# Performance work log

Hardware: AMD Instinct MI355X
Metric: run time of the kernel (lower is better)

## Reference

```python
import jax, jax.numpy as jnp
import numpy as np

N_NODES = 100000; N_RELS = 100; EMB = 128; HID = 768; LAYERS = 12
CW = 3; HEADS = 12; DH = HID // HEADS; FF = 4 * HID
B = 256; S = 128


def _statics():
    # Sliding-window mask from build_mask(): rows with offset <= S-L get the
    # submask [0]*2cw + [-inf] + [0]*2cw at [offset:offset+L]; remaining rows
    # are all -inf (we neutralize those rows to avoid NaN; their attn output
    # is zeroed, see VALID).
    Lw = 4 * CW + 1
    r = np.arange(S)[:, None]; c = np.arange(S)[None, :]
    valid = np.arange(S) <= S - Lw
    inwin = (c >= r) & (c < r + Lw) & (c != r + 2 * CW) & valid[:, None]
    addmask = np.where(inwin, 0.0, -np.inf).astype(np.float32)
    addmask = np.where(valid[:, None], addmask, 0.0)
    ri, ci = np.nonzero(inwin)  # selection indices for pos_dist[:, mask]
    # sinusoidal positional encoding (S, HID)
    pos = np.arange(S)[:, None].astype(np.float32)
    div = np.exp(-np.log(10000.0) * np.arange(0, HID, 2) / HID)
    pe = np.zeros((S, HID), np.float32)
    pe[:, 0::2] = np.sin(pos * div); pe[:, 1::2] = np.cos(pos * div)
    return (jnp.asarray(addmask), jnp.asarray(valid), jnp.asarray(ri),
            jnp.asarray(ci), jnp.asarray(pe))

ADDMASK, VALID, RI, CI, PE = _statics()


def _ln(x, g, b, eps=1e-5):
    m = jnp.mean(x, -1, keepdims=True)
    v = jnp.mean((x - m) ** 2, -1, keepdims=True)
    return (x - m) * jax.lax.rsqrt(v + eps) * g + b


def setup_inputs() -> dict:
    key = jax.random.key(0)
    ks = iter(jax.random.split(key, 40))
    nrm = lambda shp, s=0.02: jax.random.normal(next(ks), shp, jnp.float32) * s
    V = N_NODES + N_RELS
    d = {}
    d['seq'] = jax.random.randint(next(ks), (B, S), 0, V, jnp.int32)
    d['neg_idx'] = jax.random.randint(next(ks), (B, S), 0, N_NODES, jnp.int32)
    d['embed_W'] = nrm((V, EMB), 1.0)
    d['embed_g'] = jnp.ones((EMB,)); d['embed_b'] = jnp.zeros((EMB,))
    d['proj_W'] = nrm((EMB, HID)); d['proj_b'] = jnp.zeros((HID,))
    d['qkv_W'] = nrm((LAYERS, HID, 3 * HID)); d['qkv_b'] = jnp.zeros((LAYERS, 3 * HID))
    d['ao_W'] = nrm((LAYERS, HID, HID)); d['ao_b'] = jnp.zeros((LAYERS, HID))
    d['ln1_g'] = jnp.ones((LAYERS, HID)); d['ln1_b'] = jnp.zeros((LAYERS, HID))
    d['ff1_W'] = nrm((LAYERS, HID, FF)); d['ff1_b'] = jnp.zeros((LAYERS, FF))
    d['ff2_W'] = nrm((LAYERS, FF, HID)); d['ff2_b'] = jnp.zeros((LAYERS, HID))
    d['ln2_g'] = jnp.ones((LAYERS, HID)); d['ln2_b'] = jnp.zeros((LAYERS, HID))
    d['head_W'] = nrm((HID, EMB)); d['head_b'] = jnp.zeros((EMB,))
    d['head_g'] = jnp.ones((EMB,)); d['head_beta'] = jnp.zeros((EMB,))
    d['oemb_W'] = nrm((V, EMB), 1.0)
    d['oemb_g'] = jnp.ones((EMB,)); d['oemb_b'] = jnp.zeros((EMB,))
    return d


def reference(seq, neg_idx, embed_W, embed_g, embed_b, proj_W, proj_b,
              qkv_W, qkv_b, ao_W, ao_b, ln1_g, ln1_b, ff1_W, ff1_b,
              ff2_W, ff2_b, ln2_g, ln2_b, head_W, head_b, head_g, head_beta,
              oemb_W, oemb_g, oemb_b):
    b, s = seq.shape
    z = _ln(embed_W[seq], embed_g, embed_b)                 # (B,S,E)
    x = jax.nn.gelu(z @ proj_W + proj_b, approximate=False)  # (B,S,H)
    x = x + PE[None, :, :]
    vrow = VALID.astype(x.dtype)[None, None, :, None]

    def layer(x, p):
        qkv = x @ p['qw'] + p['qb']
        q, k, v = jnp.split(qkv, 3, axis=-1)
        q = q.reshape(b, s, HEADS, DH); k = k.reshape(b, s, HEADS, DH)
        v = v.reshape(b, s, HEADS, DH)
        scores = jnp.einsum('bihd,bjhd->bhij', q, k) / np.sqrt(DH)
        attn = jax.nn.softmax(scores + ADDMASK, axis=-1) * vrow
        ctx = jnp.einsum('bhij,bjhd->bihd', attn, v).reshape(b, s, HID)
        x = _ln(x + ctx @ p['aw'] + p['ab'], p['g1'], p['b1'])
        h = jax.nn.gelu(x @ p['f1w'] + p['f1b'], approximate=False)
        x = _ln(x + h @ p['f2w'] + p['f2b'], p['g2'], p['b2'])
        return x, None

    params = {'qw': qkv_W, 'qb': qkv_b, 'aw': ao_W, 'ab': ao_b,
              'g1': ln1_g, 'b1': ln1_b, 'f1w': ff1_W, 'f1b': ff1_b,
              'f2w': ff2_W, 'f2b': ff2_b, 'g2': ln2_g, 'b2': ln2_b}
    x, _ = jax.lax.scan(layer, x, params)

    preds = _ln(x @ head_W + head_b, head_g, head_beta)     # (B,S,E)
    out_z = _ln(oemb_W[seq], oemb_g, oemb_b)                # (B,S,E)
    pos_dist = jnp.einsum('bie,bje->bij', out_z, preds)     # (B,S,S)
    pos = pos_dist[:, RI, CI].reshape(-1, 2 * CW).mean(-1)
    neg_e = _ln(oemb_W[neg_idx], oemb_g, oemb_b)
    neg_dist = jnp.einsum('bie,bje->bij', out_z, neg_e)
    neg = neg_dist[:, RI, CI].reshape(-1, 2 * CW).mean(-1)
    # BCEWithLogitsLoss: labels 1 for pos, 0 for neg, mean reduction
    n = pos.shape[0] + neg.shape[0]
    loss = (jnp.sum(jax.nn.softplus(-pos)) + jnp.sum(jax.nn.softplus(neg))) / n
    return loss
```

## Files before the change

### kernel.cpp

```cpp
#include <hip/hip_runtime.h>
#include <hip/hip_bf16.h>

typedef __hip_bfloat16 bf16;
typedef __bf16 bf16x8 __attribute__((ext_vector_type(8)));
typedef float f32x4 __attribute__((ext_vector_type(4)));

#define B_      256
#define S_      128
#define HID_    768
#define EMB_    128
#define FF_     3072
#define LAYERS_ 12
#define HEADS_  12
#define DH_     64
#define M_TOK   (B_ * S_)

__device__ inline float b2f(bf16 v) { return __bfloat162float(v); }
__device__ inline bf16  f2b(float v) { return __float2bfloat16(v); }

__device__ inline float wave_sum(float v) {
#pragma unroll
  for (int o = 32; o > 0; o >>= 1) v += __shfl_xor(v, o, 64);
  return v;
}

__device__ inline float gelu_exact(float x) {
  return 0.5f * x * (1.0f + erff(x * 0.70710678118654752f));
}

__device__ inline void glds16(const bf16* g, bf16* l) {
  __builtin_amdgcn_global_load_lds(
      (const __attribute__((address_space(1))) void*)g,
      (__attribute__((address_space(3))) void*)l, 16, 0, 0);
}

__device__ inline void bar()   { asm volatile("s_barrier" ::: "memory"); }
__device__ inline void lgkm0() {
  asm volatile("s_waitcnt lgkmcnt(0)" ::: "memory");
  __builtin_amdgcn_sched_barrier(0);
}

__global__ __launch_bounds__(512, 2)
void gemm256(const bf16* __restrict__ A, const bf16* __restrict__ Bt,
             const float* __restrict__ bias, bf16* __restrict__ C,
             int M, int N, int K, int mode)
{
  __shared__ __align__(16) bf16 As[2][256 * 64];
  __shared__ __align__(16) bf16 Bs[2][256 * 64];
  const int tid  = threadIdx.x;
  const int w    = tid >> 6, lane = tid & 63;
  const int wm   = w >> 2,  wn   = w & 3;

  const int nwg = gridDim.x * gridDim.y;
  int bid = blockIdx.y * gridDim.x + blockIdx.x;
  {
    const int q = nwg >> 3, r = nwg & 7, xcd = bid & 7, off = bid >> 3;
    bid = (xcd < r ? xcd * (q + 1) : r * (q + 1) + (xcd - r) * q) + off;
  }
  const int m0 = (bid / gridDim.x) * 256;
  const int n0 = (bid % gridDim.x) * 256;

  const int NT = K >> 6;

  const int c0   = w * 2;
  const int srow = c0 * 8 + (lane >> 3);
  const int scol = ((lane & 7) ^ (lane >> 3)) * 8;
  const bf16* gA0 = A  + (size_t)(m0 + srow)     * K + scol;
  const bf16* gA1 = A  + (size_t)(m0 + srow + 8) * K + scol;
  const bf16* gB0 = Bt + (size_t)(n0 + srow)     * K + scol;
  const bf16* gB1 = Bt + (size_t)(n0 + srow + 8) * K + scol;

  auto stageA = [&](int bi, int h, int kt) {
    const size_t go = (size_t)h * 128 * (size_t)K + (size_t)kt * 64;
    bf16* l = &As[bi][h * 8192 + c0 * 512];
    glds16(gA0 + go, l);
    glds16(gA1 + go, l + 512);
  };
  auto stageB = [&](int bi, int h, int kt) {
    const size_t go = (size_t)h * 128 * (size_t)K + (size_t)kt * 64;
    bf16* l = &Bs[bi][h * 8192 + c0 * 512];
    glds16(gB0 + go, l);
    glds16(gB1 + go, l + 512);
  };

  const int lr = lane & 15, lk = (lane >> 4) * 8, sx = (lane & 7) << 3;
  auto rdA = [&](int bi, int f, int kk) -> bf16x8 {
    return *(const bf16x8*)&As[bi][((f * 32 + wm * 16 + lr) * 64 + kk * 32 + lk) ^ sx];
  };
  auto rdB = [&](int bi, int g, int kk) -> bf16x8 {
    return *(const bf16x8*)&Bs[bi][((g * 64 + wn * 16 + lr) * 64 + kk * 32 + lk) ^ sx];
  };

  const f32x4 zacc = {0.f, 0.f, 0.f, 0.f};
  f32x4 acc[8][4];
#pragma unroll
  for (int f = 0; f < 8; f++)
#pragma unroll
    for (int g = 0; g < 4; g++) acc[f][g] = zacc;

  stageA(0, 0, 0);
  stageB(0, 1, 0);
  stageB(0, 0, 0);
  stageA(0, 1, 0);
  if (NT > 1) { stageA(1, 0, 1); stageB(1, 1, 1); }
  asm volatile("s_waitcnt vmcnt(4)" ::: "memory");
  bar();

  for (int kt = 0; kt < NT; ++kt) {
    const int bi = kt & 1, nb = bi ^ 1;
    bf16x8 af[4][2], b01[2][2], b23[2][2];

#pragma unroll
    for (int f = 0; f < 4; f++) { af[f][0] = rdA(bi, f, 0); af[f][1] = rdA(bi, f, 1); }
#pragma unroll
    for (int g = 0; g < 2; g++) { b01[g][0] = rdB(bi, g, 0); b01[g][1] = rdB(bi, g, 1); }
    if (kt + 1 < NT) stageB(nb, 0, kt + 1);
    bar(); lgkm0();
    __builtin_amdgcn_s_setprio(1);
#pragma unroll
    for (int f = 0; f < 4; f++)
#pragma unroll
      for (int g = 0; g < 2; g++) {
        acc[f][g] = __builtin_amdgcn_mfma_f32_16x16x32_bf16(af[f][0], b01[g][0], acc[f][g], 0, 0, 0);
        acc[f][g] = __builtin_amdgcn_mfma_f32_16x16x32_bf16(af[f][1], b01[g][1], acc[f][g], 0, 0, 0);
      }
    __builtin_amdgcn_s_setprio(0);
    bar();

#pragma unroll
    for (int g = 0; g < 2; g++) { b23[g][0] = rdB(bi, g + 2, 0); b23[g][1] = rdB(bi, g + 2, 1); }
    if (kt + 1 < NT) stageA(nb, 1, kt + 1);
    bar(); lgkm0();
    __builtin_amdgcn_s_setprio(1);
#pragma unroll
    for (int f = 0; f < 4; f++)
#pragma unroll
      for (int g = 0; g < 2; g++) {
        acc[f][g + 2] = __builtin_amdgcn_mfma_f32_16x16x32_bf16(af[f][0], b23[g][0], acc[f][g + 2], 0, 0, 0);
        acc[f][g + 2] = __builtin_amdgcn_mfma_f32_16x16x32_bf16(af[f][1], b23[g][1], acc[f][g + 2], 0, 0, 0);
      }
    __builtin_amdgcn_s_setprio(0);
    bar();

#pragma unroll
    for (int f = 0; f < 4; f++) { af[f][0] = rdA(bi, f + 4, 0); af[f][1] = rdA(bi, f + 4, 1); }
    if (kt + 2 < NT) stageA(bi, 0, kt + 2);
    bar(); lgkm0();
    __builtin_amdgcn_s_setprio(1);
#pragma unroll
    for (int f = 0; f < 4; f++)
#pragma unroll
      for (int g = 0; g < 2; g++) {
        acc[f + 4][g + 2] = __builtin_amdgcn_mfma_f32_16x16x32_bf16(af[f][0], b23[g][0], acc[f + 4][g + 2], 0, 0, 0);
        acc[f + 4][g + 2] = __builtin_amdgcn_mfma_f32_16x16x32_bf16(af[f][1], b23[g][1], acc[f + 4][g + 2], 0, 0, 0);
      }
    __builtin_amdgcn_s_setprio(0);
    bar();

    if (kt + 2 < NT) stageB(bi, 1, kt + 2);
    if (kt < NT - 2) asm volatile("s_waitcnt vmcnt(4)" ::: "memory");
    else             asm volatile("s_waitcnt vmcnt(0)" ::: "memory");
    bar();
    __builtin_amdgcn_s_setprio(1);
#pragma unroll
    for (int f = 0; f < 4; f++)
#pragma unroll
      for (int g = 0; g < 2; g++) {
        acc[f + 4][g] = __builtin_amdgcn_mfma_f32_16x16x32_bf16(af[f][0], b01[g][0], acc[f + 4][g], 0, 0, 0);
        acc[f + 4][g] = __builtin_amdgcn_mfma_f32_16x16x32_bf16(af[f][1], b01[g][1], acc[f + 4][g], 0, 0, 0);
      }
    __builtin_amdgcn_s_setprio(0);
    bar();
  }

  const int er = (lane >> 4) * 4, ec = lane & 15;
#pragma unroll
  for (int f = 0; f < 8; f++) {
    const int row = m0 + f * 32 + wm * 16 + er;
#pragma unroll
    for (int g = 0; g < 4; g++) {
      const int col = n0 + g * 64 + wn * 16 + ec;
      const float bv = bias[col];
#pragma unroll
      for (int r = 0; r < 4; r++) {
        float v = acc[f][g][r] + bv;
        if (mode >= 1) v = gelu_exact(v);
        C[(size_t)(row + r) * N + col] = f2b(v);
      }
    }
  }
}

__global__ __launch_bounds__(256)
void gemm_bt(const bf16* __restrict__ A, const bf16* __restrict__ Bt,
             const float* __restrict__ bias, bf16* __restrict__ C,
             int M, int N, int K, int mode)
{
  __shared__ __align__(16) bf16 As[128 * 32];
  __shared__ __align__(16) bf16 Bs[128 * 32];
  const int tid  = threadIdx.x;
  const int wave = tid >> 6, lane = tid & 63;
  const int m0 = blockIdx.y * 128, n0 = blockIdx.x * 128;

  const int ar = lane >> 2;
  const int ac = (lane & 3) * 8;
  const int c0 = wave * 2;
  const bf16* ga0 = A  + (size_t)(m0 + c0 * 16      + ar) * K + ac;
  const bf16* ga1 = A  + (size_t)(m0 + (c0+1) * 16  + ar) * K + ac;
  const bf16* gb0 = Bt + (size_t)(n0 + c0 * 16      + ar) * K + ac;
  const bf16* gb1 = Bt + (size_t)(n0 + (c0+1) * 16  + ar) * K + ac;
  bf16* lA0 = As + c0 * 512;       bf16* lA1 = As + (c0 + 1) * 512;
  bf16* lB0 = Bs + c0 * 512;       bf16* lB1 = Bs + (c0 + 1) * 512;

  const int lr = lane & 15;
  const int lk = (lane >> 4) * 8;
  const int rm = (wave >> 1) * 64;
  const int rn = (wave & 1) * 64;

  const f32x4 zacc = {0.f, 0.f, 0.f, 0.f};
  f32x4 acc[4][4];
#pragma unroll
  for (int i = 0; i < 4; i++)
#pragma unroll
    for (int j = 0; j < 4; j++) acc[i][j] = zacc;

  for (int k0 = 0; k0 < K; k0 += 32) {
    glds16(ga0 + k0, lA0);
    glds16(ga1 + k0, lA1);
    glds16(gb0 + k0, lB0);
    glds16(gb1 + k0, lB1);
    __syncthreads();
    bf16x8 af[4], bfr[4];
#pragma unroll
    for (int i = 0; i < 4; i++) af[i]  = *(const bf16x8*)&As[(rm + i * 16 + lr) * 32 + lk];
#pragma unroll
    for (int j = 0; j < 4; j++) bfr[j] = *(const bf16x8*)&Bs[(rn + j * 16 + lr) * 32 + lk];
#pragma unroll
    for (int i = 0; i < 4; i++)
#pragma unroll
      for (int j = 0; j < 4; j++)
        acc[i][j] = __builtin_amdgcn_mfma_f32_16x16x32_bf16(af[i], bfr[j], acc[i][j], 0, 0, 0);
    __syncthreads();
  }

  const int er = (lane >> 4) * 4;
  const int ec = lane & 15;
#pragma unroll
  for (int i = 0; i < 4; i++) {
    const int row = m0 + rm + i * 16 + er;
#pragma unroll
    for (int j = 0; j < 4; j++) {
      const int col = n0 + rn + j * 16 + ec;
      const float bv = bias[col];
#pragma unroll
      for (int r = 0; r < 4; r++) {
        float v = acc[i][j][r] + bv;
        if (mode >= 1) v = gelu_exact(v);
        if (mode == 2) {
          const int srow = (row + r) & (S_ - 1);
          const int i2 = col & ~1;
          const float div = expf(-9.210340371976184f * (float)i2 * (1.0f / (float)HID_));
          const float ang = (float)srow * div;
          v += (col & 1) ? cosf(ang) : sinf(ang);
        }
        C[(size_t)(row + r) * N + col] = f2b(v);
      }
    }
  }
}

__global__ __launch_bounds__(256)
void convtrans(const float* __restrict__ src, bf16* __restrict__ dst, int K, int N)
{
  __shared__ bf16 t[32][33];
  const int n0 = blockIdx.x * 32, k0 = blockIdx.y * 32;
  const int tx = threadIdx.x, ty = threadIdx.y;
#pragma unroll
  for (int i = 0; i < 4; i++)
    t[ty + i * 8][tx] = f2b(src[(size_t)(k0 + ty + i * 8) * N + n0 + tx]);
  __syncthreads();
#pragma unroll
  for (int i = 0; i < 4; i++)
    dst[(size_t)(n0 + ty + i * 8) * K + k0 + tx] = t[tx][ty + i * 8];
}

__global__ __launch_bounds__(128)
void attn_kernel(const bf16* __restrict__ qkv, bf16* __restrict__ ctx)
{
  const int bh = blockIdx.x;
  const int b = bh / HEADS_, h = bh % HEADS_;
  __shared__ __align__(16) bf16 qs[S_ * DH_];
  __shared__ __align__(16) bf16 ks[S_ * DH_];
  __shared__ __align__(16) bf16 vs[S_ * DH_];
  const int tid = threadIdx.x;
  const bf16* base = qkv + (size_t)b * S_ * (3 * HID_) + h * DH_;
  for (int it = 0; it < 8; ++it) {
    const int s = it * 16 + (tid >> 3);
    const int seg = (tid & 7) * 8;
    const size_t go = (size_t)s * (3 * HID_) + seg;
    *(uint4*)&qs[s * DH_ + seg] = *(const uint4*)&base[go];
    *(uint4*)&ks[s * DH_ + seg] = *(const uint4*)&base[go + HID_];
    *(uint4*)&vs[s * DH_ + seg] = *(const uint4*)&base[go + 2 * HID_];
  }
  __syncthreads();
  const int i = tid;
  bf16* out = ctx + (size_t)(b * S_ + i) * HID_ + h * DH_;
  if (i < 116) {
    float p[13];
    float mx = -1e30f;
    for (int jj = 0; jj < 13; jj++) {
      if (jj == 6) { p[jj] = 0.f; continue; }
      float d = 0.f;
#pragma unroll
      for (int dd = 0; dd < DH_; dd++) d += b2f(qs[i * DH_ + dd]) * b2f(ks[(i + jj) * DH_ + dd]);
      p[jj] = d * 0.125f;
      mx = fmaxf(mx, p[jj]);
    }
    float l = 0.f;
    for (int jj = 0; jj < 13; jj++) {
      if (jj == 6) { p[jj] = 0.f; continue; }
      p[jj] = expf(p[jj] - mx);
      l += p[jj];
    }
    const float inv = 1.f / l;
    float o[DH_];
#pragma unroll
    for (int dd = 0; dd < DH_; dd++) o[dd] = 0.f;
    for (int jj = 0; jj < 13; jj++) {
      if (jj == 6) continue;
      const float pj = p[jj] * inv;
#pragma unroll
      for (int dd = 0; dd < DH_; dd++) o[dd] += pj * b2f(vs[(i + jj) * DH_ + dd]);
    }
#pragma unroll
    for (int dd = 0; dd < DH_; dd++) out[dd] = f2b(o[dd]);
  } else {
#pragma unroll
    for (int dd = 0; dd < DH_; dd++) out[dd] = f2b(0.f);
  }
}

__global__ __launch_bounds__(256)
void add_ln_kernel(const bf16* __restrict__ x, const bf16* __restrict__ y,
                   const float* __restrict__ g, const float* __restrict__ bta,
                   bf16* __restrict__ out)
{
  const int r = blockIdx.x, tid = threadIdx.x;
  const size_t base = (size_t)r * HID_;
  float v[3];
#pragma unroll
  for (int e = 0; e < 3; e++) {
    const int idx = tid + e * 256;
    v[e] = b2f(x[base + idx]) + b2f(y[base + idx]);
  }
  float s  = v[0] + v[1] + v[2];
  float ss = v[0] * v[0] + v[1] * v[1] + v[2] * v[2];
  s = wave_sum(s);
  ss = wave_sum(ss);
  __shared__ float red[8];
  const int wave = tid >> 6, lane = tid & 63;
  if (lane == 0) { red[wave] = s; red[4 + wave] = ss; }
  __syncthreads();
  s  = red[0] + red[1] + red[2] + red[3];
  ss = red[4] + red[5] + red[6] + red[7];
  const float mean = s * (1.f / (float)HID_);
  const float var  = ss * (1.f / (float)HID_) - mean * mean;
  const float rs = rsqrtf(var + 1e-5f);
#pragma unroll
  for (int e = 0; e < 3; e++) {
    const int idx = tid + e * 256;
    out[base + idx] = f2b((v[e] - mean) * rs * g[idx] + bta[idx]);
  }
}

__global__ __launch_bounds__(256)
void gather_ln128(const int* __restrict__ idx, const float* __restrict__ W,
                  const float* __restrict__ g, const float* __restrict__ bta,
                  bf16* __restrict__ out)
{
  const int token = blockIdx.x * 4 + (threadIdx.x >> 6);
  const int lane = threadIdx.x & 63;
  const int row = idx[token];
  const float* src = W + (size_t)row * 128;
  const float a = src[lane], c = src[lane + 64];
  const float s  = wave_sum(a + c);
  const float ss = wave_sum(a * a + c * c);
  const float mean = s * (1.f / 128.f);
  const float var  = ss * (1.f / 128.f) - mean * mean;
  const float rs = rsqrtf(var + 1e-5f);
  bf16* o = out + (size_t)token * 128;
  o[lane]      = f2b((a - mean) * rs * g[lane] + bta[lane]);
  o[lane + 64] = f2b((c - mean) * rs * g[lane + 64] + bta[lane + 64]);
}

__global__ __launch_bounds__(256)
void ln128_bf16(const bf16* __restrict__ in, const float* __restrict__ g,
                const float* __restrict__ bta, bf16* __restrict__ out)
{
  const int token = blockIdx.x * 4 + (threadIdx.x >> 6);
  const int lane = threadIdx.x & 63;
  const bf16* src = in + (size_t)token * 128;
  const float a = b2f(src[lane]), c = b2f(src[lane + 64]);
  const float s  = wave_sum(a + c);
  const float ss = wave_sum(a * a + c * c);
  const float mean = s * (1.f / 128.f);
  const float var  = ss * (1.f / 128.f) - mean * mean;
  const float rs = rsqrtf(var + 1e-5f);
  bf16* o = out + (size_t)token * 128;
  o[lane]      = f2b((a - mean) * rs * g[lane] + bta[lane]);
  o[lane + 64] = f2b((c - mean) * rs * g[lane + 64] + bta[lane + 64]);
}

__global__ __launch_bounds__(256)
void loss_kernel(const bf16* __restrict__ out_z, const bf16* __restrict__ preds,
                 const bf16* __restrict__ neg_e, float* __restrict__ out)
{
  const int b = blockIdx.x;
  const int which = blockIdx.y;
  __shared__ __align__(16) bf16 zo[128 * 128];
  __shared__ __align__(16) bf16 mt[128 * 128];
  const bf16* msrc = which ? neg_e : preds;
  const uint4* gz = (const uint4*)(out_z + (size_t)b * 16384);
  const uint4* gm = (const uint4*)(msrc + (size_t)b * 16384);
  for (int it = threadIdx.x; it < 2048; it += 256) {
    ((uint4*)zo)[it] = gz[it];
    ((uint4*)mt)[it] = gm[it];
  }
  __syncthreads();
  float local = 0.f;
  for (int it = threadIdx.x; it < 232; it += 256) {
    const int i = it >> 1;
    const int sub = it & 1;
    const int c0 = i + (sub ? 7 : 0);
    const bf16* zr = &zo[i * 128];
    float accv = 0.f;
    for (int jj = 0; jj < 6; jj++) {
      const bf16* mr = &mt[(c0 + jj) * 128];
      float d = 0.f;
#pragma unroll
      for (int dd = 0; dd < 128; dd++) d += b2f(zr[dd]) * b2f(mr[dd]);
      accv += d;
    }
    const float mean = accv * (1.f / 6.f);
    const float xin = which ? mean : -mean;
    local += fmaxf(xin, 0.f) + log1pf(expf(-fabsf(xin)));
  }
  local = wave_sum(local);
  if ((threadIdx.x & 63) == 0)
    atomicAdd(out, local * (1.f / 118784.f));
}

__global__ void zero_kernel(float* p) { p[0] = 0.f; }

extern "C" void kernel_launch(void* const* d_in, const int* in_sizes, int n_in,
                              void* d_out, int out_size, void* d_ws, size_t ws_size,
                              hipStream_t stream)
{
  (void)in_sizes; (void)n_in; (void)out_size; (void)ws_size;
  const int*   seq     = (const int*)  d_in[0];
  const int*   neg_idx = (const int*)  d_in[1];
  const float* embed_W = (const float*)d_in[2];
  const float* embed_g = (const float*)d_in[3];
  const float* embed_b = (const float*)d_in[4];
  const float* proj_W  = (const float*)d_in[5];
  const float* proj_b  = (const float*)d_in[6];
  const float* qkv_W   = (const float*)d_in[7];
  const float* qkv_b   = (const float*)d_in[8];
  const float* ao_W    = (const float*)d_in[9];
  const float* ao_b    = (const float*)d_in[10];
  const float* ln1_g   = (const float*)d_in[11];
  const float* ln1_b   = (const float*)d_in[12];
  const float* ff1_W   = (const float*)d_in[13];
  const float* ff1_b   = (const float*)d_in[14];
  const float* ff2_W   = (const float*)d_in[15];
  const float* ff2_b   = (const float*)d_in[16];
  const float* ln2_g   = (const float*)d_in[17];
  const float* ln2_b   = (const float*)d_in[18];
  const float* head_W  = (const float*)d_in[19];
  const float* head_b  = (const float*)d_in[20];
  const float* head_g  = (const float*)d_in[21];
  const float* head_bt = (const float*)d_in[22];
  const float* oemb_W  = (const float*)d_in[23];
  const float* oemb_g  = (const float*)d_in[24];
  const float* oemb_b  = (const float*)d_in[25];
  float* out = (float*)d_out;

  char* ws = (char*)d_ws;
  size_t off = 0;
  auto alloc = [&](size_t bytes) -> char* {
    char* p = ws + off;
    off += (bytes + 255) & ~(size_t)255;
    return p;
  };
  bf16* wt_qkv  = (bf16*)alloc((size_t)2304 * 768 * 2);
  bf16* wt_ao   = (bf16*)alloc((size_t)768 * 768 * 2);
  bf16* wt_ff1  = (bf16*)alloc((size_t)3072 * 768 * 2);
  bf16* wt_ff2  = (bf16*)alloc((size_t)768 * 3072 * 2);
  bf16* wt_proj = (bf16*)alloc((size_t)768 * 128 * 2);
  bf16* wt_head = (bf16*)alloc((size_t)128 * 768 * 2);
  bf16* zbuf    = (bf16*)alloc((size_t)M_TOK * 128 * 2);
  bf16* x       = (bf16*)alloc((size_t)M_TOK * 768 * 2);
  bf16* big     = (bf16*)alloc((size_t)M_TOK * 3072 * 2);
  bf16* ctx     = (bf16*)alloc((size_t)M_TOK * 768 * 2);
  bf16* ybuf    = (bf16*)alloc((size_t)M_TOK * 768 * 2);
  bf16* p0      = (bf16*)alloc((size_t)M_TOK * 128 * 2);
  bf16* preds   = (bf16*)alloc((size_t)M_TOK * 128 * 2);
  bf16* outz    = (bf16*)alloc((size_t)M_TOK * 128 * 2);
  bf16* nege    = (bf16*)alloc((size_t)M_TOK * 128 * 2);

  const dim3 tb(32, 8);

  convtrans<<<dim3(768 / 32, 128 / 32), tb, 0, stream>>>(proj_W, wt_proj, 128, 768);
  convtrans<<<dim3(128 / 32, 768 / 32), tb, 0, stream>>>(head_W, wt_head, 768, 128);

  gather_ln128<<<M_TOK / 4, 256, 0, stream>>>(seq, embed_W, embed_g, embed_b, zbuf);
  gemm_bt<<<dim3(768 / 128, M_TOK / 128), 256, 0, stream>>>(zbuf, wt_proj, proj_b, x,
                                                            M_TOK, 768, 128, 2);

  for (int l = 0; l < LAYERS_; ++l) {
    convtrans<<<dim3(2304 / 32, 768 / 32), tb, 0, stream>>>(qkv_W + (size_t)l * 768 * 2304, wt_qkv, 768, 2304);
    convtrans<<<dim3(768 / 32, 768 / 32), tb, 0, stream>>>(ao_W + (size_t)l * 768 * 768, wt_ao, 768, 768);
    convtrans<<<dim3(3072 / 32, 768 / 32), tb, 0, stream>>>(ff1_W + (size_t)l * 768 * 3072, wt_ff1, 768, 3072);
    convtrans<<<dim3(768 / 32, 3072 / 32), tb, 0, stream>>>(ff2_W + (size_t)l * 3072 * 768, wt_ff2, 3072, 768);

    gemm256<<<dim3(2304 / 256, M_TOK / 256), 512, 0, stream>>>(x, wt_qkv, qkv_b + l * 2304, big,
                                                               M_TOK, 2304, 768, 0);
    attn_kernel<<<B_ * HEADS_, 128, 0, stream>>>(big, ctx);
    gemm256<<<dim3(768 / 256, M_TOK / 256), 512, 0, stream>>>(ctx, wt_ao, ao_b + l * 768, ybuf,
                                                              M_TOK, 768, 768, 0);
    add_ln_kernel<<<M_TOK, 256, 0, stream>>>(x, ybuf, ln1_g + l * 768, ln1_b + l * 768, x);
    gemm256<<<dim3(3072 / 256, M_TOK / 256), 512, 0, stream>>>(x, wt_ff1, ff1_b + l * 3072, big,
                                                               M_TOK, 3072, 768, 1);
    gemm256<<<dim3(768 / 256, M_TOK / 256), 512, 0, stream>>>(big, wt_ff2, ff2_b + l * 768, ybuf,
                                                              M_TOK, 768, 3072, 0);
    add_ln_kernel<<<M_TOK, 256, 0, stream>>>(x, ybuf, ln2_g + l * 768, ln2_b + l * 768, x);
  }

  gemm_bt<<<dim3(1, M_TOK / 128), 256, 0, stream>>>(x, wt_head, head_b, p0, M_TOK, 128, 768, 0);
  ln128_bf16<<<M_TOK / 4, 256, 0, stream>>>(p0, head_g, head_bt, preds);
  gather_ln128<<<M_TOK / 4, 256, 0, stream>>>(seq, oemb_W, oemb_g, oemb_b, outz);
  gather_ln128<<<M_TOK / 4, 256, 0, stream>>>(neg_idx, oemb_W, oemb_g, oemb_b, nege);
  zero_kernel<<<1, 1, 0, stream>>>(out);
  loss_kernel<<<dim3(B_, 2), 256, 0, stream>>>(outz, preds, nege, out);
}
```

Before: 10.71 ms.

## Make GEMM persistent with cross-tile prefetch and use polynomial GELU approximation

Turns the 256x256 GEMM into a persistent kernel of 256 workgroups, each looping over several output tiles. The next tile's first k-slices are prefetched while the current tile finishes, so the pipeline does not drain between tiles, and launch tail effects shrink. It also replaces erff-based exact GELU with an Abramowitz-Stegun polynomial plus fast exp, which cuts epilogue cost but adds approximation error of roughly 1e-7 in erf. The tile split assumes the tile count divides evenly by 8 XCDs and 32 slots per XCD.

```diff
diff --git a/kernel.cpp b/kernel.cpp
--- a/kernel.cpp
+++ b/kernel.cpp
@@ -24,8 +24,19 @@
   return v;
 }
 
-__device__ inline float gelu_exact(float x) {
-  return 0.5f * x * (1.0f + erff(x * 0.70710678118654752f));
+__device__ inline float gelu_fast(float x) {
+  const float s  = x * 0.70710678118654752f;
+  const float ax = fabsf(s);
+  const float t  = 1.0f / fmaf(0.3275911f, ax, 1.0f);
+  float y = fmaf(t, 1.061405429f, -1.453152027f);
+  y = fmaf(t, y, 1.421413741f);
+  y = fmaf(t, y, -0.284496736f);
+  y = fmaf(t, y, 0.254829592f);
+  y = y * t;
+  const float e  = __expf(-ax * ax);
+  float er = 1.0f - y * e;
+  er = copysignf(er, s);
+  return 0.5f * x * (1.0f + er);
 }
 
 __device__ inline void glds16(const bf16* g, bf16* l) {
@@ -41,9 +52,9 @@
 }
 
 __global__ __launch_bounds__(512, 2)
-void gemm256(const bf16* __restrict__ A, const bf16* __restrict__ Bt,
-             const float* __restrict__ bias, bf16* __restrict__ C,
-             int M, int N, int K, int mode)
+void gemm256p(const bf16* __restrict__ A, const bf16* __restrict__ Bt,
+              const float* __restrict__ bias, bf16* __restrict__ C,
+              int M, int N, int K, int mode)
 {
   __shared__ __align__(16) bf16 As[2][256 * 64];
   __shared__ __align__(16) bf16 Bs[2][256 * 64];
@@ -51,36 +62,36 @@
   const int w    = tid >> 6, lane = tid & 63;
   const int wm   = w >> 2,  wn   = w & 3;
 
-  const int nwg = gridDim.x * gridDim.y;
-  int bid = blockIdx.y * gridDim.x + blockIdx.x;
-  {
-    const int q = nwg >> 3, r = nwg & 7, xcd = bid & 7, off = bid >> 3;
-    bid = (xcd < r ? xcd * (q + 1) : r * (q + 1) + (xcd - r) * q) + off;
-  }
-  const int m0 = (bid / gridDim.x) * 256;
-  const int n0 = (bid % gridDim.x) * 256;
-
+  const int gx  = N >> 8;
+  const int T   = (M >> 8) * gx;
+  const int Cx  = T >> 3;
+  const int xcd = blockIdx.x & 7, ci = blockIdx.x >> 3;
+  if (ci >= Cx) return;
+  const int R = (Cx - 1 - ci) / 32 + 1;
   const int NT = K >> 6;
+  const int U  = R * NT;
+
+  int jc = 0, kt = 0;
+  const int t0 = xcd * Cx + ci;
+  int m0 = (t0 / gx) << 8, n0 = (t0 % gx) << 8;
+  int m0n = 0, n0n = 0;
+  if (R > 1) { const int tn = t0 + 32; m0n = (tn / gx) << 8; n0n = (tn % gx) << 8; }
 
   const int c0   = w * 2;
   const int srow = c0 * 8 + (lane >> 3);
   const int scol = ((lane & 7) ^ (lane >> 3)) * 8;
-  const bf16* gA0 = A  + (size_t)(m0 + srow)     * K + scol;
-  const bf16* gA1 = A  + (size_t)(m0 + srow + 8) * K + scol;
-  const bf16* gB0 = Bt + (size_t)(n0 + srow)     * K + scol;
-  const bf16* gB1 = Bt + (size_t)(n0 + srow + 8) * K + scol;
-
-  auto stageA = [&](int bi, int h, int kt) {
-    const size_t go = (size_t)h * 128 * (size_t)K + (size_t)kt * 64;
+
+  auto stA = [&](int bi, int h, int m0t, int ktt) {
+    const bf16* g = A + (size_t)(m0t + h * 128 + srow) * K + (ktt * 64 + scol);
     bf16* l = &As[bi][h * 8192 + c0 * 512];
-    glds16(gA0 + go, l);
-    glds16(gA1 + go, l + 512);
+    glds16(g, l);
+    glds16(g + (size_t)8 * K, l + 512);
   };
-  auto stageB = [&](int bi, int h, int kt) {
-    const size_t go = (size_t)h * 128 * (size_t)K + (size_t)kt * 64;
+  auto stB = [&](int bi, int h, int n0t, int ktt) {
+    const bf16* g = Bt + (size_t)(n0t + h * 128 + srow) * K + (ktt * 64 + scol);
     bf16* l = &Bs[bi][h * 8192 + c0 * 512];
-    glds16(gB0 + go, l);
-    glds16(gB1 + go, l + 512);
+    glds16(g, l);
+    glds16(g + (size_t)8 * K, l + 512);
   };
 
   const int lr = lane & 15, lk = (lane >> 4) * 8, sx = (lane & 7) << 3;
@@ -98,23 +109,28 @@
 #pragma unroll
     for (int g = 0; g < 4; g++) acc[f][g] = zacc;
 
-  stageA(0, 0, 0);
-  stageB(0, 1, 0);
-  stageB(0, 0, 0);
-  stageA(0, 1, 0);
-  if (NT > 1) { stageA(1, 0, 1); stageB(1, 1, 1); }
+  const int er = (lane >> 4) * 4, ec = lane & 15;
+
+  stA(0, 0, m0, 0); stB(0, 1, n0, 0); stB(0, 0, n0, 0); stA(0, 1, m0, 0);
+  stA(1, 0, m0, 1); stB(1, 1, n0, 1);
   asm volatile("s_waitcnt vmcnt(4)" ::: "memory");
   bar();
 
-  for (int kt = 0; kt < NT; ++kt) {
-    const int bi = kt & 1, nb = bi ^ 1;
+  for (int u = 0; u < U; ++u) {
+    const int bi = u & 1, nb = bi ^ 1;
+    const bool h1 = (u + 1 < U), h2 = (u + 2 < U);
+    int kt1 = kt + 1, m01 = m0, n01 = n0;
+    if (kt1 == NT) { kt1 = 0; m01 = m0n; n01 = n0n; }
+    int kt2 = kt + 2, m02 = m0, n02 = n0;
+    if (kt2 >= NT) { kt2 -= NT; m02 = m0n; n02 = n0n; }
+
     bf16x8 af[4][2], b01[2][2], b23[2][2];
 
 #pragma unroll
     for (int f = 0; f < 4; f++) { af[f][0] = rdA(bi, f, 0); af[f][1] = rdA(bi, f, 1); }
 #pragma unroll
     for (int g = 0; g < 2; g++) { b01[g][0] = rdB(bi, g, 0); b01[g][1] = rdB(bi, g, 1); }
-    if (kt + 1 < NT) stageB(nb, 0, kt + 1);
+    if (h1) stB(nb, 0, n01, kt1);
     bar(); lgkm0();
     __builtin_amdgcn_s_setprio(1);
 #pragma unroll
@@ -129,7 +145,7 @@
 
 #pragma unroll
     for (int g = 0; g < 2; g++) { b23[g][0] = rdB(bi, g + 2, 0); b23[g][1] = rdB(bi, g + 2, 1); }
-    if (kt + 1 < NT) stageA(nb, 1, kt + 1);
+    if (h1) stA(nb, 1, m01, kt1);
     bar(); lgkm0();
     __builtin_amdgcn_s_setprio(1);
 #pragma unroll
@@ -144,7 +160,7 @@
 
 #pragma unroll
     for (int f = 0; f < 4; f++) { af[f][0] = rdA(bi, f + 4, 0); af[f][1] = rdA(bi, f + 4, 1); }
-    if (kt + 2 < NT) stageA(bi, 0, kt + 2);
+    if (h2) stA(bi, 0, m02, kt2);
     bar(); lgkm0();
     __builtin_amdgcn_s_setprio(1);
 #pragma unroll
@@ -157,9 +173,9 @@
     __builtin_amdgcn_s_setprio(0);
     bar();
 
-    if (kt + 2 < NT) stageB(bi, 1, kt + 2);
-    if (kt < NT - 2) asm volatile("s_waitcnt vmcnt(4)" ::: "memory");
-    else             asm volatile("s_waitcnt vmcnt(0)" ::: "memory");
+    if (h2) stB(bi, 1, n02, kt2);
+    if (u < U - 2) asm volatile("s_waitcnt vmcnt(4)" ::: "memory");
+    else           asm volatile("s_waitcnt vmcnt(0)" ::: "memory");
     bar();
     __builtin_amdgcn_s_setprio(1);
 #pragma unroll
@@ -171,21 +187,29 @@
       }
     __builtin_amdgcn_s_setprio(0);
     bar();
-  }
-
-  const int er = (lane >> 4) * 4, ec = lane & 15;
-#pragma unroll
-  for (int f = 0; f < 8; f++) {
-    const int row = m0 + f * 32 + wm * 16 + er;
-#pragma unroll
-    for (int g = 0; g < 4; g++) {
-      const int col = n0 + g * 64 + wn * 16 + ec;
-      const float bv = bias[col];
-#pragma unroll
-      for (int r = 0; r < 4; r++) {
-        float v = acc[f][g][r] + bv;
-        if (mode >= 1) v = gelu_exact(v);
-        C[(size_t)(row + r) * N + col] = f2b(v);
+
+    if (++kt == NT) {
+#pragma unroll
+      for (int f = 0; f < 8; f++) {
+        const int row = m0 + f * 32 + wm * 16 + er;
+#pragma unroll
+        for (int g = 0; g < 4; g++) {
+          const int col = n0 + g * 64 + wn * 16 + ec;
+          const float bv = bias[col];
+#pragma unroll
+          for (int r = 0; r < 4; r++) {
+            float v = acc[f][g][r] + bv;
+            if (mode >= 1) v = gelu_fast(v);
+            C[(size_t)(row + r) * N + col] = f2b(v);
+          }
+          acc[f][g] = zacc;
+        }
+      }
+      kt = 0; ++jc;
+      m0 = m0n; n0 = n0n;
+      if (jc + 1 < R) {
+        const int tn = xcd * Cx + (jc + 1) * 32 + ci;
+        m0n = (tn / gx) << 8; n0n = (tn % gx) << 8;
       }
     }
   }
@@ -255,7 +279,7 @@
 #pragma unroll
       for (int r = 0; r < 4; r++) {
         float v = acc[i][j][r] + bv;
-        if (mode >= 1) v = gelu_exact(v);
+        if (mode >= 1) v = gelu_fast(v);
         if (mode == 2) {
           const int srow = (row + r) & (S_ - 1);
           const int i2 = col & ~1;
@@ -523,16 +547,12 @@
     convtrans<<<dim3(3072 / 32, 768 / 32), tb, 0, stream>>>(ff1_W + (size_t)l * 768 * 3072, wt_ff1, 768, 3072);
     convtrans<<<dim3(768 / 32, 3072 / 32), tb, 0, stream>>>(ff2_W + (size_t)l * 3072 * 768, wt_ff2, 3072, 768);
 
-    gemm256<<<dim3(2304 / 256, M_TOK / 256), 512, 0, stream>>>(x, wt_qkv, qkv_b + l * 2304, big,
-                                                               M_TOK, 2304, 768, 0);
+    gemm256p<<<256, 512, 0, stream>>>(x, wt_qkv, qkv_b + l * 2304, big, M_TOK, 2304, 768, 0);
     attn_kernel<<<B_ * HEADS_, 128, 0, stream>>>(big, ctx);
-    gemm256<<<dim3(768 / 256, M_TOK / 256), 512, 0, stream>>>(ctx, wt_ao, ao_b + l * 768, ybuf,
-                                                              M_TOK, 768, 768, 0);
+    gemm256p<<<256, 512, 0, stream>>>(ctx, wt_ao, ao_b + l * 768, ybuf, M_TOK, 768, 768, 0);
     add_ln_kernel<<<M_TOK, 256, 0, stream>>>(x, ybuf, ln1_g + l * 768, ln1_b + l * 768, x);
-    gemm256<<<dim3(3072 / 256, M_TOK / 256), 512, 0, stream>>>(x, wt_ff1, ff1_b + l * 3072, big,
-                                                               M_TOK, 3072, 768, 1);
-    gemm256<<<dim3(768 / 256, M_TOK / 256), 512, 0, stream>>>(big, wt_ff2, ff2_b + l * 768, ybuf,
-                                                              M_TOK, 768, 3072, 0);
+    gemm256p<<<256, 512, 0, stream>>>(x, wt_ff1, ff1_b + l * 3072, big, M_TOK, 3072, 768, 1);
+    gemm256p<<<256, 512, 0, stream>>>(big, wt_ff2, ff2_b + l * 768, ybuf, M_TOK, 768, 3072, 0);
     add_ln_kernel<<<M_TOK, 256, 0, stream>>>(x, ybuf, ln2_g + l * 768, ln2_b + l * 768, x);
   }
 
```

Result: faster. 10.32 ms (-3.6%).
